# Optimization experiments

Measured on AMD Instinct MI355X. Metric: run time of the kernel, lower is better.

Reference implementation:

```python
import jax, jax.numpy as jnp
import numpy as np

N = 1000        # genomes
S = 32          # samples
M = 2_000_000   # total genes
K = 100_000     # sequences (contigs)


def setup_inputs() -> dict:
    key = jax.random.key(0)
    k1, k2, k3, k4, k5 = jax.random.split(key, 5)
    A = jax.random.normal(k1, (N, S), dtype=jnp.float32)          # log-abundance
    B = jax.random.uniform(k2, (N, S), dtype=jnp.float32)         # log-PTR in [0,1]
    pos = jax.random.uniform(k3, (M,), dtype=jnp.float32)         # gene position in [0,1]
    genome_idx = jax.random.randint(k4, (M,), 0, N)               # one-hot column of `members`
    seq_idx = jax.random.randint(k5, (M,), 0, K)                  # row of `gene_to_seq`
    return {"A": A, "B": B, "pos": pos, "genome_idx": genome_idx, "seq_idx": seq_idx}


def reference(A, B, pos, genome_idx, seq_idx):
    # G = members @ A + 1 - dists @ B  ==  A[g] + 1 - pos * B[g] per gene  -> [M, S]
    G = A[genome_idx] + 1.0 - pos[:, None] * B[genome_idx]
    # E @ exp(G): sum exp(G) over genes belonging to each sequence -> [K, S]
    return jax.ops.segment_sum(jnp.exp(G), seq_idx, num_segments=K)
```

## Files before the change

### kernel.cpp

```cpp
#include <hip/hip_runtime.h>
#include <hip/hip_bf16.h>


#define CHUNK 8192
#define NBMAX 1024
#define CAPLG 12
#define CAP   (1 << CAPLG)
#define SCAP  3072

__device__ inline float fast_exp2(float x) {
    float r;
    asm("v_exp_f32 %0, %1" : "=v"(r) : "v"(x));
    return r;
}

__global__ __launch_bounds__(256) void prep_kernel(
    const float* __restrict__ A, const float* __restrict__ B,
    unsigned* __restrict__ AB2p, int* __restrict__ gcur, int NS)
{
    const int i = blockIdx.x * 256 + threadIdx.x;
    if (i < NBMAX) gcur[i] = 0;
    if (i >= NS) return;
    const float a2 = (A[i] + 1.0f) * 1.44269504f;
    const float b2 = B[i] * (1.44269504f / 32768.0f);
    const _Float16 ha = (_Float16)a2;
    const unsigned short ua = __builtin_bit_cast(unsigned short, ha);
    unsigned bb = __float_as_uint(b2);
    bb = (bb + 0x7FFFu + ((bb >> 16) & 1u)) & 0xFFFF0000u;
    AB2p[i] = (unsigned)ua | bb;
}

__global__ __launch_bounds__(1024) void partition_kernel(
    const float* __restrict__ pos, const int* __restrict__ gidx,
    const int* __restrict__ sidx, int* __restrict__ gcur,
    unsigned* __restrict__ payload, int M, int NB)
{
    __shared__ int h[NBMAX];
    __shared__ int pfx[NBMAX];
    __shared__ int dbase[NBMAX];
    __shared__ int wsum[16];
    __shared__ unsigned stg_p[CHUNK];
    const int t = threadIdx.x, blk = blockIdx.x;
    const int i0 = blk * CHUNK;
    const int n = min(CHUNK, M - i0);
    const int l16 = t & 15, grp16 = t >> 4;

    h[t] = 0;
    __syncthreads();

    unsigned pl[8];
    int bb[8], rk[8];
#pragma unroll
    for (int u = 0; u < 8; u++) {
        const int j = t + u * 1024;
        rk[u] = -1;
        if (j < n) {
            const int sx = sidx[i0 + j];
            const int b = sx >> 7;
            const float p = pos[i0 + j];
            int q = (int)fmaf(p, 32768.0f, 0.5f);
            q = min(q, 32767);
            pl[u] = (unsigned)(sx & 127)
                  | ((unsigned)gidx[i0 + j] << 7)
                  | ((unsigned)q << 17);
            bb[u] = b;
            rk[u] = atomicAdd(&h[b], 1);
        }
    }
    __syncthreads();

    {
        const int v = h[t];
        int incl = v;
#pragma unroll
        for (int d = 1; d < 64; d <<= 1) {
            const int x = __shfl_up(incl, d);
            if ((t & 63) >= d) incl += x;
        }
        if ((t & 63) == 63) wsum[t >> 6] = incl;
        __syncthreads();
        if (t < 16) {
            const int wv = wsum[t];
            int winc = wv;
#pragma unroll
            for (int d = 1; d < 16; d <<= 1) {
                const int x = __shfl_up(winc, d, 16);
                if (t >= d) winc += x;
            }
            wsum[t] = winc - wv;
        }
        __syncthreads();
        pfx[t] = wsum[t >> 6] + incl - v;
    }
    __syncthreads();

#pragma unroll
    for (int u = 0; u < 8; u++)
        if (rk[u] >= 0) stg_p[pfx[bb[u]] + rk[u]] = pl[u];

    if (t < NB) {
        const int hc = h[t];
        int dst = t << CAPLG;
        if (hc > 0) dst += atomicAdd(&gcur[t], hc);
        dbase[t] = dst;
    }
    __syncthreads();

    for (int b = grp16; b < NB; b += 64) {
        const int cnt = h[b];
        if (cnt == 0) continue;
        const int src = pfx[b];
        const int dst = dbase[b];
        for (int i = l16; i < cnt; i += 16) {
            const int rr = dst + i;
            if ((rr >> CAPLG) == b) payload[rr] = stg_p[src + i];
        }
    }
}

__global__ __launch_bounds__(512) void fused_reduce_kernel(
    const unsigned* __restrict__ AB2p, const unsigned* __restrict__ payload,
    const int* __restrict__ gcur, float* __restrict__ out, int K)
{
    __shared__ unsigned sorted[SCAP + 8];
    __shared__ int hw[8][64];
    __shared__ int wb[8][64];
    __shared__ int h[64], pfx[64];
    const int t = threadIdx.x;
    const int bkt = blockIdx.x >> 1;
    const int sp  = blockIdx.x & 1;
    const int g4  = (t >> 4) & 3;
    const int l16 = t & 15;
    const unsigned lane8 = (unsigned)(l16 << 3);
    const int wv = t >> 6;
    const int start = bkt << CAPLG;
    const int n = min(gcur[bkt], CAP);

    ((int*)hw)[t] = 0;
    __syncthreads();

    unsigned r[8];
    int rk[8];
#pragma unroll
    for (int u = 0; u < 8; u++) {
        const int idx = t + u * 512;
        rk[u] = -1;
        if (idx < n) {
            const unsigned w = payload[start + idx];
            if (((w >> 6) & 1u) == (unsigned)sp) {
                r[u] = w;
                rk[u] = atomicAdd(&hw[wv][w & 63], 1);
            }
        }
    }
    __syncthreads();

    if (t < 64) {
        int run = 0;
#pragma unroll
        for (int w = 0; w < 8; w++) { wb[w][t] = run; run += hw[w][t]; }
        h[t] = run;
        int incl = run;
#pragma unroll
        for (int d = 1; d < 64; d <<= 1) {
            const int x = __shfl_up(incl, d);
            if (t >= d) incl += x;
        }
        pfx[t] = incl - run;
    }
    __syncthreads();

#pragma unroll
    for (int u = 0; u < 8; u++)
        if (rk[u] >= 0) {
            const int bin = r[u] & 63;
            const int d = pfx[bin] + wb[wv][bin] + rk[u];
            if (d < SCAP) sorted[d] = r[u];
        }
    __syncthreads();

#define GPROC(gi, A0, A1)                                                     \
    {                                                                         \
        const unsigned w = sorted[gi];                                        \
        const bool valid = (gi) < e;                                          \
        const unsigned voff = (w & 0x1FF80u) | lane8;                         \
        const uint2 ab = *(const uint2*)((const char*)AB2p + voff);           \
        const float qf = (float)(w >> 17);                                    \
        float fa0, fa1;                                                       \
        asm("v_cvt_f32_f16 %0, %1" : "=v"(fa0) : "v"(ab.x));                  \
        asm("v_cvt_f32_f16 %0, %1" : "=v"(fa1) : "v"(ab.y));                  \
        float x0 = fmaf(-qf, __int_as_float(ab.x & 0xFFFF0000u), fa0);        \
        float x1 = fmaf(-qf, __int_as_float(ab.y & 0xFFFF0000u), fa1);        \
        x0 = valid ? x0 : -2000.0f;                                           \
        x1 = valid ? x1 : -2000.0f;                                           \
        A0 += fast_exp2(x0);                                                  \
        A1 += fast_exp2(x1);                                                  \
    }

    const int seqbase = (bkt << 7) + (sp << 6) + (wv << 3);
    for (int q = 0; q < 8; q++) {
        const int ls = (wv << 3) + q;
        const int i0 = pfx[ls];
        const int e = min(i0 + h[ls], SCAP);
        float a0 = 0.0f, a1 = 0.0f, b0 = 0.0f, b1 = 0.0f;
        int i = i0;
        for (; i + 4 < e; i += 8) {
            GPROC(i + g4, a0, a1);
            GPROC(i + 4 + g4, b0, b1);
        }
        for (; i < e; i += 4)
            GPROC(i + g4, a0, a1);
        float acc0 = a0 + b0, acc1 = a1 + b1;
        acc0 += __shfl_xor(acc0, 16);
        acc1 += __shfl_xor(acc1, 16);
        acc0 += __shfl_xor(acc0, 32);
        acc1 += __shfl_xor(acc1, 32);
        const int seq = seqbase + q;
        if ((t & 48) == 0 && seq < K)
            *(float2*)&out[(seq << 5) + (l16 << 1)] = make_float2(acc0, acc1);
    }
#undef GPROC
}

__global__ __launch_bounds__(256) void scatter_exp_fallback(
    const float* __restrict__ A, const float* __restrict__ B,
    const float* __restrict__ pos, const int* __restrict__ gidx,
    const int* __restrict__ sidx, float* __restrict__ out, int M)
{
    const int lane = threadIdx.x & 31;
    int group = (int)((blockIdx.x * blockDim.x + threadIdx.x) >> 5);
    const int stride = (int)((gridDim.x * blockDim.x) >> 5);
    for (int g = group; g < M; g += stride) {
        const int gi = gidx[g];
        const int si = sidx[g];
        const float p = pos[g];
        const float a = A[(gi << 5) + lane];
        const float b = B[(gi << 5) + lane];
        atomicAdd(&out[(si << 5) + lane], __expf(fmaf(-p, b, a + 1.0f)));
    }
}

extern "C" void kernel_launch(void* const* d_in, const int* in_sizes, int n_in,
                              void* d_out, int out_size, void* d_ws, size_t ws_size,
                              hipStream_t stream)
{
    const float* A    = (const float*)d_in[0];
    const float* B    = (const float*)d_in[1];
    const float* pos  = (const float*)d_in[2];
    const int*   gidx = (const int*)d_in[3];
    const int*   sidx = (const int*)d_in[4];
    float*       out  = (float*)d_out;

    const int M  = in_sizes[2];
    const int NS = in_sizes[0];
    const int N  = NS / 32;
    const int K  = out_size / 32;
    const int NB = (K + 127) >> 7;
    const int NBLK = (M + CHUNK - 1) / CHUNK;

    char* ws = (char*)d_ws;
    size_t off = 0;
    int* gcur = (int*)(ws + off);       off += (size_t)NBMAX * sizeof(int);
    off = (off + 255) & ~(size_t)255;
    unsigned* AB2p = (unsigned*)(ws + off); off += (size_t)N * 32 * sizeof(unsigned);
    off = (off + 255) & ~(size_t)255;
    unsigned* payload = (unsigned*)(ws + off);
    const size_t need = off + ((size_t)NB << CAPLG) * sizeof(unsigned);

    const bool packable = (NB <= NBMAX) && (K <= NBMAX * 128) && (N <= 1024)
                       && (M / (NB > 0 ? NB : 1) <= CAP / 4 * 3);
    if (!packable || ws_size < need) {
        hipMemsetAsync(d_out, 0, (size_t)out_size * sizeof(float), stream);
        scatter_exp_fallback<<<8192, 256, 0, stream>>>(A, B, pos, gidx, sidx, out, M);
        return;
    }

    const int prep_grid = (max(NS, NBMAX) + 255) / 256;
    prep_kernel     <<<prep_grid, 256, 0, stream>>>(A, B, AB2p, gcur, NS);
    partition_kernel<<<NBLK, 1024, 0, stream>>>(pos, gidx, sidx, gcur, payload, M, NB);
    fused_reduce_kernel<<<NB * 2, 512, 0, stream>>>(AB2p, payload, gcur, out, K);
}
```

Baseline: 58.44 us.

## Split reduce into four quarter-bucket blocks of 256 threads with vectorized payload loads

The fused reduce kernel now launches four 256-thread blocks per bucket instead of two 512-thread blocks. Each block handles 32 sequences, which drops the per-wave histogram and the two-level prefix in favour of a single 32-bin shared atomic histogram. Payload is read with uint4 loads. Each block must still read the whole bucket's payload, so global reads double in exchange for more blocks, lower shared memory and higher occupancy. Shared atomic contention on 32 bins across all waves may increase.

```diff
diff --git a/kernel.cpp b/kernel.cpp
--- a/kernel.cpp
+++ b/kernel.cpp
@@ -6,7 +6,7 @@
 #define NBMAX 1024
 #define CAPLG 12
 #define CAP   (1 << CAPLG)
-#define SCAP  3072
+#define QCAP  2048
 
 __device__ inline float fast_exp2(float x) {
     float r;
@@ -118,17 +118,15 @@
     }
 }
 
-__global__ __launch_bounds__(512) void fused_reduce_kernel(
+__global__ __launch_bounds__(256, 8) void fused_reduce_kernel(
     const unsigned* __restrict__ AB2p, const unsigned* __restrict__ payload,
     const int* __restrict__ gcur, float* __restrict__ out, int K)
 {
-    __shared__ unsigned sorted[SCAP + 8];
-    __shared__ int hw[8][64];
-    __shared__ int wb[8][64];
-    __shared__ int h[64], pfx[64];
+    __shared__ unsigned sorted[QCAP + 8];
+    __shared__ int h[32], pfx[32];
     const int t = threadIdx.x;
-    const int bkt = blockIdx.x >> 1;
-    const int sp  = blockIdx.x & 1;
+    const int bkt = blockIdx.x >> 2;
+    const int qt  = blockIdx.x & 3;
     const int g4  = (t >> 4) & 3;
     const int l16 = t & 15;
     const unsigned lane8 = (unsigned)(l16 << 3);
@@ -136,56 +134,54 @@
     const int start = bkt << CAPLG;
     const int n = min(gcur[bkt], CAP);
 
-    ((int*)hw)[t] = 0;
-    __syncthreads();
-
-    unsigned r[8];
-    int rk[8];
-#pragma unroll
-    for (int u = 0; u < 8; u++) {
-        const int idx = t + u * 512;
-        rk[u] = -1;
-        if (idx < n) {
-            const unsigned w = payload[start + idx];
-            if (((w >> 6) & 1u) == (unsigned)sp) {
-                r[u] = w;
-                rk[u] = atomicAdd(&hw[wv][w & 63], 1);
-            }
-        }
-    }
-    __syncthreads();
-
-    if (t < 64) {
-        int run = 0;
-#pragma unroll
-        for (int w = 0; w < 8; w++) { wb[w][t] = run; run += hw[w][t]; }
-        h[t] = run;
-        int incl = run;
-#pragma unroll
-        for (int d = 1; d < 64; d <<= 1) {
-            const int x = __shfl_up(incl, d);
+    if (t < 32) h[t] = 0;
+    __syncthreads();
+
+    unsigned w[16];
+    int rk[16];
+#pragma unroll
+    for (int u = 0; u < 4; u++) {
+        const int e4 = (u * 256 + t) * 4;
+        const uint4 v = *(const uint4*)(payload + start + e4);
+        w[4 * u] = v.x; w[4 * u + 1] = v.y; w[4 * u + 2] = v.z; w[4 * u + 3] = v.w;
+#pragma unroll
+        for (int j = 0; j < 4; j++) {
+            const int s = 4 * u + j;
+            const unsigned ww = w[s];
+            rk[s] = -1;
+            if (e4 + j < n && (int)((ww >> 5) & 3u) == qt)
+                rk[s] = atomicAdd(&h[ww & 31], 1);
+        }
+    }
+    __syncthreads();
+
+    if (t < 32) {
+        const int v = h[t];
+        int incl = v;
+#pragma unroll
+        for (int d = 1; d < 32; d <<= 1) {
+            const int x = __shfl_up(incl, d, 32);
             if (t >= d) incl += x;
         }
-        pfx[t] = incl - run;
-    }
-    __syncthreads();
-
-#pragma unroll
-    for (int u = 0; u < 8; u++)
-        if (rk[u] >= 0) {
-            const int bin = r[u] & 63;
-            const int d = pfx[bin] + wb[wv][bin] + rk[u];
-            if (d < SCAP) sorted[d] = r[u];
+        pfx[t] = incl - v;
+    }
+    __syncthreads();
+
+#pragma unroll
+    for (int s = 0; s < 16; s++)
+        if (rk[s] >= 0) {
+            const int d = pfx[w[s] & 31] + rk[s];
+            if (d < QCAP) sorted[d] = w[s];
         }
     __syncthreads();
 
 #define GPROC(gi, A0, A1)                                                     \
     {                                                                         \
-        const unsigned w = sorted[gi];                                        \
+        const unsigned ww = sorted[gi];                                       \
         const bool valid = (gi) < e;                                          \
-        const unsigned voff = (w & 0x1FF80u) | lane8;                         \
+        const unsigned voff = (ww & 0x1FF80u) | lane8;                        \
         const uint2 ab = *(const uint2*)((const char*)AB2p + voff);           \
-        const float qf = (float)(w >> 17);                                    \
+        const float qf = (float)(ww >> 17);                                   \
         float fa0, fa1;                                                       \
         asm("v_cvt_f32_f16 %0, %1" : "=v"(fa0) : "v"(ab.x));                  \
         asm("v_cvt_f32_f16 %0, %1" : "=v"(fa1) : "v"(ab.y));                  \
@@ -197,11 +193,11 @@
         A1 += fast_exp2(x1);                                                  \
     }
 
-    const int seqbase = (bkt << 7) + (sp << 6) + (wv << 3);
+    const int seqbase = (bkt << 7) + (qt << 5) + (wv << 3);
     for (int q = 0; q < 8; q++) {
         const int ls = (wv << 3) + q;
         const int i0 = pfx[ls];
-        const int e = min(i0 + h[ls], SCAP);
+        const int e = min(i0 + h[ls], QCAP);
         float a0 = 0.0f, a1 = 0.0f, b0 = 0.0f, b1 = 0.0f;
         int i = i0;
         for (; i + 4 < e; i += 8) {
@@ -278,5 +274,5 @@
     const int prep_grid = (max(NS, NBMAX) + 255) / 256;
     prep_kernel     <<<prep_grid, 256, 0, stream>>>(A, B, AB2p, gcur, NS);
     partition_kernel<<<NBLK, 1024, 0, stream>>>(pos, gidx, sidx, gcur, payload, M, NB);
-    fused_reduce_kernel<<<NB * 2, 512, 0, stream>>>(AB2p, payload, gcur, out, K);
-}
+    fused_reduce_kernel<<<NB * 4, 256, 0, stream>>>(AB2p, payload, gcur, out, K);
+}
```

After: 59.17 us. Within noise of the previous version (+1.2%).
